# Kernel tuning notes

Measured on AMD Instinct MI355X. Metric: run time of the kernel, lower is better.

## Reference

```python
import jax, jax.numpy as jnp
import numpy as np

B, STATE, OBS = 131072, 16, 8


def _spd(key, b, n, scale=0.1):
    a = jax.random.normal(key, (b, n, n), dtype=jnp.float32) * scale
    return a @ jnp.swapaxes(a, -1, -2) + jnp.eye(n, dtype=jnp.float32)


def setup_inputs() -> dict:
    key = jax.random.key(0)
    ks = jax.random.split(key, 7)
    return {
        "input": jax.random.normal(ks[0], (B, OBS), dtype=jnp.float32),
        "mean": jax.random.normal(ks[1], (B, STATE), dtype=jnp.float32),
        "cov": _spd(ks[2], B, STATE),
        "H": jax.random.normal(ks[3], (B, OBS, STATE), dtype=jnp.float32) * 0.3,
        "R": _spd(ks[4], B, OBS),
        "F": jax.random.normal(ks[5], (B, STATE, STATE), dtype=jnp.float32) * 0.1,
        "Q": _spd(ks[6], B, STATE),
    }


def reference(input, mean, cov, H, R, F, Q):
    # ---- update (no NaNs in input, so the full-batch path is taken) ----
    Ht = jnp.swapaxes(H, -1, -2)                      # [B, s, o]
    S = H @ cov @ Ht + R                              # system covariance [B, o, o]
    PHt = cov @ Ht                                    # [B, s, o]
    # torch.solve(B, A) solves A X = B with A = S^T, B = (cov H^T)^T; K = X^T
    Kt = jnp.linalg.solve(jnp.swapaxes(S, -1, -2), jnp.swapaxes(PHt, -1, -2))
    K = jnp.swapaxes(Kt, -1, -2)                      # Kalman gain [B, s, o]
    resid = input - jnp.einsum('bos,bs->bo', H, mean)  # innovation [B, o]
    new_mean = mean + jnp.einsum('bso,bo->bs', K, resid)
    # Joseph-stabilized covariance update
    I = jnp.eye(cov.shape[-1], dtype=cov.dtype)
    p1 = I - K @ H                                    # [B, s, s]
    new_cov = p1 @ cov @ jnp.swapaxes(p1, -1, -2) + K @ R @ jnp.swapaxes(K, -1, -2)
    # ---- predict ----
    pred_mean = jnp.einsum('bij,bj->bi', F, new_mean)
    pred_cov = F @ new_cov @ jnp.swapaxes(F, -1, -2) + Q
    return pred_mean, pred_cov
```

## Files before the change

### kernel.cpp

```cpp
#include <hip/hip_runtime.h>
#include <math.h>


#define NB 131072
#define BPB 4
#define THREADS 64
#define LDS_PER 616

#define ROW_FMA16(acc, s, base) do {                                        \
    const float4* _r = (const float4*)(base);                               \
    float4 _c0=_r[0], _c1=_r[1], _c2=_r[2], _c3=_r[3];                      \
    acc[0]+=(s)*_c0.x; acc[1]+=(s)*_c0.y; acc[2]+=(s)*_c0.z; acc[3]+=(s)*_c0.w; \
    acc[4]+=(s)*_c1.x; acc[5]+=(s)*_c1.y; acc[6]+=(s)*_c1.z; acc[7]+=(s)*_c1.w; \
    acc[8]+=(s)*_c2.x; acc[9]+=(s)*_c2.y; acc[10]+=(s)*_c2.z; acc[11]+=(s)*_c2.w; \
    acc[12]+=(s)*_c3.x; acc[13]+=(s)*_c3.y; acc[14]+=(s)*_c3.z; acc[15]+=(s)*_c3.w; \
} while (0)

#define ROW_FMA8(acc, s, base) do {                                         \
    const float4* _r = (const float4*)(base);                               \
    float4 _c0=_r[0], _c1=_r[1];                                            \
    acc[0]+=(s)*_c0.x; acc[1]+=(s)*_c0.y; acc[2]+=(s)*_c0.z; acc[3]+=(s)*_c0.w; \
    acc[4]+=(s)*_c1.x; acc[5]+=(s)*_c1.y; acc[6]+=(s)*_c1.z; acc[7]+=(s)*_c1.w; \
} while (0)

__global__ void __launch_bounds__(THREADS, 4)
kalman_step_kernel(const float* __restrict__ input, const float* __restrict__ mean,
                   const float* __restrict__ cov, const float* __restrict__ H,
                   const float* __restrict__ R, const float* __restrict__ F,
                   const float* __restrict__ Q,
                   float* __restrict__ out_mean, float* __restrict__ out_cov)
{
    __shared__ __align__(16) float lds[BPB * LDS_PER];

    const int tid = threadIdx.x;
    const int g = tid >> 4;
    const int t = tid & 15;
    const long b = (long)blockIdx.x * BPB + g;

    float* Lb    = lds + g * LDS_PER;
    float* Mb    = Lb;
    float* Hb    = Lb + 256;
    float* Rb    = Lb + 384;
    float* Xb    = Lb + 448;
    float* meanv = Lb + 576;
    float* rn    = Lb + 592;

    float covrow[16];
    {
        const float4* C4 = (const float4*)(cov + b * 256 + t * 16);
        float4 c0 = C4[0], c1 = C4[1], c2 = C4[2], c3 = C4[3];
        covrow[0]=c0.x; covrow[1]=c0.y; covrow[2]=c0.z; covrow[3]=c0.w;
        covrow[4]=c1.x; covrow[5]=c1.y; covrow[6]=c1.z; covrow[7]=c1.w;
        covrow[8]=c2.x; covrow[9]=c2.y; covrow[10]=c2.z; covrow[11]=c2.w;
        covrow[12]=c3.x; covrow[13]=c3.y; covrow[14]=c3.z; covrow[15]=c3.w;
        float4* md = (float4*)(Mb + t * 16);
        md[0]=c0; md[1]=c1; md[2]=c2; md[3]=c3;
    }
    const float m = mean[b * 16 + t];
    meanv[t] = m;

    float hreg[16];
    float rreg[8];
    float inp = 0.0f;
    if (t < 8) {
        inp = input[b * 8 + t];
        const float4* H4 = (const float4*)(H + b * 128 + t * 16);
        float4 h0 = H4[0], h1 = H4[1], h2 = H4[2], h3 = H4[3];
        hreg[0]=h0.x; hreg[1]=h0.y; hreg[2]=h0.z; hreg[3]=h0.w;
        hreg[4]=h1.x; hreg[5]=h1.y; hreg[6]=h1.z; hreg[7]=h1.w;
        hreg[8]=h2.x; hreg[9]=h2.y; hreg[10]=h2.z; hreg[11]=h2.w;
        hreg[12]=h3.x; hreg[13]=h3.y; hreg[14]=h3.z; hreg[15]=h3.w;
        float4* hd = (float4*)(Hb + t * 16);
        hd[0]=h0; hd[1]=h1; hd[2]=h2; hd[3]=h3;
        const float4* R4 = (const float4*)(R + b * 64 + t * 8);
        float4 r0 = R4[0], r1 = R4[1];
        rreg[0]=r0.x; rreg[1]=r0.y; rreg[2]=r0.z; rreg[3]=r0.w;
        rreg[4]=r1.x; rreg[5]=r1.y; rreg[6]=r1.z; rreg[7]=r1.w;
        float4* rd = (float4*)(Rb + t * 8);
        rd[0]=r0; rd[1]=r1;
    }
    __syncthreads();

    float pht[8];
    #pragma unroll
    for (int o = 0; o < 8; ++o) {
        const float4* hr = (const float4*)(Hb + o * 16);
        float4 h0 = hr[0], h1 = hr[1], h2 = hr[2], h3 = hr[3];
        float acc;
        acc  = covrow[0]*h0.x + covrow[1]*h0.y + covrow[2]*h0.z + covrow[3]*h0.w;
        acc += covrow[4]*h1.x + covrow[5]*h1.y + covrow[6]*h1.z + covrow[7]*h1.w;
        acc += covrow[8]*h2.x + covrow[9]*h2.y + covrow[10]*h2.z + covrow[11]*h2.w;
        acc += covrow[12]*h3.x + covrow[13]*h3.y + covrow[14]*h3.z + covrow[15]*h3.w;
        pht[o] = acc;
    }
    {
        float4* pd = (float4*)(Xb + t * 8);
        pd[0] = make_float4(pht[0], pht[1], pht[2], pht[3]);
        pd[1] = make_float4(pht[4], pht[5], pht[6], pht[7]);
    }
    if (t < 8) {
        const float4* mv = (const float4*)meanv;
        float4 m0 = mv[0], m1 = mv[1], m2 = mv[2], m3 = mv[3];
        float acc = inp;
        acc -= hreg[0]*m0.x + hreg[1]*m0.y + hreg[2]*m0.z + hreg[3]*m0.w;
        acc -= hreg[4]*m1.x + hreg[5]*m1.y + hreg[6]*m1.z + hreg[7]*m1.w;
        acc -= hreg[8]*m2.x + hreg[9]*m2.y + hreg[10]*m2.z + hreg[11]*m2.w;
        acc -= hreg[12]*m3.x + hreg[13]*m3.y + hreg[14]*m3.z + hreg[15]*m3.w;
        rn[t] = acc;
    }
    __syncthreads();

    if (t < 8) {
        float sreg[8];
        #pragma unroll
        for (int c = 0; c < 8; ++c) sreg[c] = rreg[c];
        #pragma unroll
        for (int s = 0; s < 16; ++s) {
            float h = hreg[s];
            ROW_FMA8(sreg, h, Xb + s * 8);
        }
        float4* sd = (float4*)(Xb + t * 8);
        sd[0] = make_float4(sreg[0], sreg[1], sreg[2], sreg[3]);
        sd[1] = make_float4(sreg[4], sreg[5], sreg[6], sreg[7]);
    }
    __syncthreads();

    float Lm[8][8];
    #pragma unroll
    for (int i = 0; i < 8; ++i) {
        const float4* sr = (const float4*)(Xb + i * 8);
        float4 s0 = sr[0], s1 = sr[1];
        Lm[i][0]=s0.x; Lm[i][1]=s0.y; Lm[i][2]=s0.z; Lm[i][3]=s0.w;
        Lm[i][4]=s1.x; Lm[i][5]=s1.y; Lm[i][6]=s1.z; Lm[i][7]=s1.w;
    }
    float dinv[8];
    #pragma unroll
    for (int k = 0; k < 8; ++k) {
        float diag = Lm[k][k];
        #pragma unroll
        for (int j = 0; j < k; ++j) diag -= Lm[k][j] * Lm[k][j];
        float lkk = sqrtf(diag);
        float inv = 1.0f / lkk;
        dinv[k] = inv;
        #pragma unroll
        for (int i = k + 1; i < 8; ++i) {
            float v = Lm[i][k];
            #pragma unroll
            for (int j = 0; j < k; ++j) v -= Lm[i][j] * Lm[k][j];
            Lm[i][k] = v * inv;
        }
    }
    float yv[8];
    #pragma unroll
    for (int i = 0; i < 8; ++i) {
        float v = pht[i];
        #pragma unroll
        for (int j = 0; j < i; ++j) v -= Lm[i][j] * yv[j];
        yv[i] = v * dinv[i];
    }
    float Kr[8];
    #pragma unroll
    for (int i = 7; i >= 0; --i) {
        float v = yv[i];
        #pragma unroll
        for (int j = i + 1; j < 8; ++j) v -= Lm[j][i] * Kr[j];
        Kr[i] = v * dinv[i];
    }
    {
        const float4* rv = (const float4*)rn;
        float4 r0 = rv[0], r1 = rv[1];
        float nm = m;
        nm += Kr[0]*r0.x + Kr[1]*r0.y + Kr[2]*r0.z + Kr[3]*r0.w;
        nm += Kr[4]*r1.x + Kr[5]*r1.y + Kr[6]*r1.z + Kr[7]*r1.w;
        rn[t] = nm;
    }
    #pragma unroll
    for (int o = 0; o < 8; ++o) Xb[o * 16 + t] = Kr[o];
    __syncthreads();

    const float4* F4 = (const float4*)(F + b * 256 + t * 16);
    float4 fA = F4[0], fB = F4[1], fC = F4[2], fD = F4[3];

    float p1r[16];
    #pragma unroll
    for (int j = 0; j < 16; ++j) p1r[j] = (j == t) ? 1.0f : 0.0f;
    #pragma unroll
    for (int o = 0; o < 8; ++o) {
        float nko = -Kr[o];
        ROW_FMA16(p1r, nko, Hb + o * 16);
    }
    float KRr[8];
    #pragma unroll
    for (int c = 0; c < 8; ++c) KRr[c] = 0.0f;
    #pragma unroll
    for (int o = 0; o < 8; ++o) {
        float ko = Kr[o];
        ROW_FMA8(KRr, ko, Rb + o * 8);
    }

    float tmp[16];
    #pragma unroll
    for (int k = 0; k < 16; ++k) tmp[k] = 0.0f;
    #pragma unroll
    for (int j = 0; j < 16; ++j) {
        float pj = p1r[j];
        ROW_FMA16(tmp, pj, Mb + j * 16);
    }
    __syncthreads();
    #pragma unroll
    for (int k = 0; k < 16; ++k) Mb[k * 16 + t] = tmp[k];
    __syncthreads();

    const float4* Q4 = (const float4*)(Q + b * 256 + t * 16);
    float4 qA = Q4[0], qB = Q4[1], qC = Q4[2], qD = Q4[3];

    float nc[16];
    #pragma unroll
    for (int j = 0; j < 16; ++j) nc[j] = 0.0f;
    #pragma unroll
    for (int k = 0; k < 16; ++k) {
        float pk = p1r[k];
        ROW_FMA16(nc, pk, Mb + k * 16);
    }
    #pragma unroll
    for (int o = 0; o < 8; ++o) {
        float ko = KRr[o];
        ROW_FMA16(nc, ko, Xb + o * 16);
    }
    __syncthreads();
    {
        float4* md = (float4*)(Mb + t * 16);
        md[0] = make_float4(nc[0], nc[1], nc[2], nc[3]);
        md[1] = make_float4(nc[4], nc[5], nc[6], nc[7]);
        md[2] = make_float4(nc[8], nc[9], nc[10], nc[11]);
        md[3] = make_float4(nc[12], nc[13], nc[14], nc[15]);
    }
    __syncthreads();

    float freg[16];
    freg[0]=fA.x; freg[1]=fA.y; freg[2]=fA.z; freg[3]=fA.w;
    freg[4]=fB.x; freg[5]=fB.y; freg[6]=fB.z; freg[7]=fB.w;
    freg[8]=fC.x; freg[9]=fC.y; freg[10]=fC.z; freg[11]=fC.w;
    freg[12]=fD.x; freg[13]=fD.y; freg[14]=fD.z; freg[15]=fD.w;

    float fp[16];
    #pragma unroll
    for (int k = 0; k < 16; ++k) fp[k] = 0.0f;
    #pragma unroll
    for (int j = 0; j < 16; ++j) {
        float fj = freg[j];
        ROW_FMA16(fp, fj, Mb + j * 16);
    }
    float pm;
    {
        const float4* rv = (const float4*)rn;
        float4 r0 = rv[0], r1 = rv[1], r2 = rv[2], r3 = rv[3];
        pm  = freg[0]*r0.x + freg[1]*r0.y + freg[2]*r0.z + freg[3]*r0.w;
        pm += freg[4]*r1.x + freg[5]*r1.y + freg[6]*r1.z + freg[7]*r1.w;
        pm += freg[8]*r2.x + freg[9]*r2.y + freg[10]*r2.z + freg[11]*r2.w;
        pm += freg[12]*r3.x + freg[13]*r3.y + freg[14]*r3.z + freg[15]*r3.w;
    }
    __syncthreads();
    #pragma unroll
    for (int k = 0; k < 16; ++k) Mb[k * 16 + t] = fp[k];
    __syncthreads();

    float pc[16];
    pc[0]=qA.x; pc[1]=qA.y; pc[2]=qA.z; pc[3]=qA.w;
    pc[4]=qB.x; pc[5]=qB.y; pc[6]=qB.z; pc[7]=qB.w;
    pc[8]=qC.x; pc[9]=qC.y; pc[10]=qC.z; pc[11]=qC.w;
    pc[12]=qD.x; pc[13]=qD.y; pc[14]=qD.z; pc[15]=qD.w;
    #pragma unroll
    for (int k = 0; k < 16; ++k) {
        float fk = freg[k];
        ROW_FMA16(pc, fk, Mb + k * 16);
    }

    out_mean[b * 16 + t] = pm;
    {
        float4* od = (float4*)(out_cov + b * 256 + t * 16);
        od[0] = make_float4(pc[0], pc[1], pc[2], pc[3]);
        od[1] = make_float4(pc[4], pc[5], pc[6], pc[7]);
        od[2] = make_float4(pc[8], pc[9], pc[10], pc[11]);
        od[3] = make_float4(pc[12], pc[13], pc[14], pc[15]);
    }
}

extern "C" void kernel_launch(void* const* d_in, const int* in_sizes, int n_in,
                              void* d_out, int out_size, void* d_ws, size_t ws_size,
                              hipStream_t stream) {
    const float* input = (const float*)d_in[0];
    const float* mean  = (const float*)d_in[1];
    const float* cov   = (const float*)d_in[2];
    const float* H     = (const float*)d_in[3];
    const float* R     = (const float*)d_in[4];
    const float* F     = (const float*)d_in[5];
    const float* Q     = (const float*)d_in[6];
    float* out = (float*)d_out;
    float* out_mean = out;
    float* out_cov  = out + (size_t)NB * 16;

    dim3 grid(NB / BPB);
    dim3 block(THREADS);
    hipLaunchKernelGGL(kalman_step_kernel, grid, block, 0, stream,
                       input, mean, cov, H, R, F, Q, out_mean, out_cov);
}
```

Before: 486.1 us.

## Fold predict into update: compute F(I-KH) directly, drop Joseph intermediate stages

The covariance math is reassociated so that G = F(I-KH) = F - (FK)H and W = FK are built first. The result is then formed as G·P·Gᵀ + W·R·Wᵀ + Q, which removes the separate Joseph-form new_cov materialization and several LDS round trips and barriers. Cov and R are no longer staged in LDS, which shrinks the per-batch footprint, and the F load is hoisted earlier to overlap with the Cholesky solve. Outputs are written with nontemporal stores, and dot products are restructured into split partial sums. The reassociation changes rounding order slightly.

Measured after the change: 523.8 us. 1.08x slower.

```diff
diff --git a/kernel.cpp b/kernel.cpp
--- a/kernel.cpp
+++ b/kernel.cpp
@@ -5,7 +5,9 @@
 #define NB 131072
 #define BPB 4
 #define THREADS 64
-#define LDS_PER 616
+#define LDS_PER 552
+
+typedef float vf4 __attribute__((ext_vector_type(4)));
 
 #define ROW_FMA16(acc, s, base) do {                                        \
     const float4* _r = (const float4*)(base);                               \
@@ -23,6 +25,24 @@
     acc[4]+=(s)*_c1.x; acc[5]+=(s)*_c1.y; acc[6]+=(s)*_c1.z; acc[7]+=(s)*_c1.w; \
 } while (0)
 
+#define DOT16(res, v, base) do {                                            \
+    const float4* _r = (const float4*)(base);                               \
+    float4 _a=_r[0], _b=_r[1], _c=_r[2], _d=_r[3];                          \
+    float _s0 = v[0]*_a.x + v[1]*_a.y + v[2]*_a.z + v[3]*_a.w;              \
+    float _s1 = v[4]*_b.x + v[5]*_b.y + v[6]*_b.z + v[7]*_b.w;              \
+    float _s2 = v[8]*_c.x + v[9]*_c.y + v[10]*_c.z + v[11]*_c.w;            \
+    float _s3 = v[12]*_d.x + v[13]*_d.y + v[14]*_d.z + v[15]*_d.w;          \
+    res = (_s0+_s1)+(_s2+_s3);                                              \
+} while (0)
+
+#define DOT8(res, v, base) do {                                             \
+    const float4* _r = (const float4*)(base);                               \
+    float4 _a=_r[0], _b=_r[1];                                              \
+    float _s0 = v[0]*_a.x + v[1]*_a.y + v[2]*_a.z + v[3]*_a.w;              \
+    float _s1 = v[4]*_b.x + v[5]*_b.y + v[6]*_b.z + v[7]*_b.w;              \
+    res = _s0 + _s1;                                                        \
+} while (0)
+
 __global__ void __launch_bounds__(THREADS, 4)
 kalman_step_kernel(const float* __restrict__ input, const float* __restrict__ mean,
                    const float* __restrict__ cov, const float* __restrict__ H,
@@ -40,10 +60,9 @@
     float* Lb    = lds + g * LDS_PER;
     float* Mb    = Lb;
     float* Hb    = Lb + 256;
-    float* Rb    = Lb + 384;
-    float* Xb    = Lb + 448;
-    float* meanv = Lb + 576;
-    float* rn    = Lb + 592;
+    float* Xb    = Lb + 384;
+    float* meanv = Lb + 512;
+    float* rn    = Lb + 528;
 
     float covrow[16];
     {
@@ -53,8 +72,6 @@
         covrow[4]=c1.x; covrow[5]=c1.y; covrow[6]=c1.z; covrow[7]=c1.w;
         covrow[8]=c2.x; covrow[9]=c2.y; covrow[10]=c2.z; covrow[11]=c2.w;
         covrow[12]=c3.x; covrow[13]=c3.y; covrow[14]=c3.z; covrow[15]=c3.w;
-        float4* md = (float4*)(Mb + t * 16);
-        md[0]=c0; md[1]=c1; md[2]=c2; md[3]=c3;
     }
     const float m = mean[b * 16 + t];
     meanv[t] = m;
@@ -76,22 +93,13 @@
         float4 r0 = R4[0], r1 = R4[1];
         rreg[0]=r0.x; rreg[1]=r0.y; rreg[2]=r0.z; rreg[3]=r0.w;
         rreg[4]=r1.x; rreg[5]=r1.y; rreg[6]=r1.z; rreg[7]=r1.w;
-        float4* rd = (float4*)(Rb + t * 8);
-        rd[0]=r0; rd[1]=r1;
     }
     __syncthreads();
 
     float pht[8];
     #pragma unroll
     for (int o = 0; o < 8; ++o) {
-        const float4* hr = (const float4*)(Hb + o * 16);
-        float4 h0 = hr[0], h1 = hr[1], h2 = hr[2], h3 = hr[3];
-        float acc;
-        acc  = covrow[0]*h0.x + covrow[1]*h0.y + covrow[2]*h0.z + covrow[3]*h0.w;
-        acc += covrow[4]*h1.x + covrow[5]*h1.y + covrow[6]*h1.z + covrow[7]*h1.w;
-        acc += covrow[8]*h2.x + covrow[9]*h2.y + covrow[10]*h2.z + covrow[11]*h2.w;
-        acc += covrow[12]*h3.x + covrow[13]*h3.y + covrow[14]*h3.z + covrow[15]*h3.w;
-        pht[o] = acc;
+        DOT16(pht[o], covrow, Hb + o * 16);
     }
     {
         float4* pd = (float4*)(Xb + t * 8);
@@ -99,14 +107,9 @@
         pd[1] = make_float4(pht[4], pht[5], pht[6], pht[7]);
     }
     if (t < 8) {
-        const float4* mv = (const float4*)meanv;
-        float4 m0 = mv[0], m1 = mv[1], m2 = mv[2], m3 = mv[3];
-        float acc = inp;
-        acc -= hreg[0]*m0.x + hreg[1]*m0.y + hreg[2]*m0.z + hreg[3]*m0.w;
-        acc -= hreg[4]*m1.x + hreg[5]*m1.y + hreg[6]*m1.z + hreg[7]*m1.w;
-        acc -= hreg[8]*m2.x + hreg[9]*m2.y + hreg[10]*m2.z + hreg[11]*m2.w;
-        acc -= hreg[12]*m3.x + hreg[13]*m3.y + hreg[14]*m3.z + hreg[15]*m3.w;
-        rn[t] = acc;
+        float hm;
+        DOT16(hm, hreg, meanv);
+        rn[t] = inp - hm;
     }
     __syncthreads();
 
@@ -125,6 +128,9 @@
     }
     __syncthreads();
 
+    const float4* F4 = (const float4*)(F + b * 256 + t * 16);
+    float4 fA = F4[0], fB = F4[1], fC = F4[2], fD = F4[3];
+
     float Lm[8][8];
     #pragma unroll
     for (int i = 0; i < 8; ++i) {
@@ -174,66 +180,10 @@
         nm += Kr[4]*r1.x + Kr[5]*r1.y + Kr[6]*r1.z + Kr[7]*r1.w;
         rn[t] = nm;
     }
-    #pragma unroll
-    for (int o = 0; o < 8; ++o) Xb[o * 16 + t] = Kr[o];
-    __syncthreads();
-
-    const float4* F4 = (const float4*)(F + b * 256 + t * 16);
-    float4 fA = F4[0], fB = F4[1], fC = F4[2], fD = F4[3];
-
-    float p1r[16];
-    #pragma unroll
-    for (int j = 0; j < 16; ++j) p1r[j] = (j == t) ? 1.0f : 0.0f;
-    #pragma unroll
-    for (int o = 0; o < 8; ++o) {
-        float nko = -Kr[o];
-        ROW_FMA16(p1r, nko, Hb + o * 16);
-    }
-    float KRr[8];
-    #pragma unroll
-    for (int c = 0; c < 8; ++c) KRr[c] = 0.0f;
-    #pragma unroll
-    for (int o = 0; o < 8; ++o) {
-        float ko = Kr[o];
-        ROW_FMA8(KRr, ko, Rb + o * 8);
-    }
-
-    float tmp[16];
-    #pragma unroll
-    for (int k = 0; k < 16; ++k) tmp[k] = 0.0f;
-    #pragma unroll
-    for (int j = 0; j < 16; ++j) {
-        float pj = p1r[j];
-        ROW_FMA16(tmp, pj, Mb + j * 16);
-    }
-    __syncthreads();
-    #pragma unroll
-    for (int k = 0; k < 16; ++k) Mb[k * 16 + t] = tmp[k];
-    __syncthreads();
-
-    const float4* Q4 = (const float4*)(Q + b * 256 + t * 16);
-    float4 qA = Q4[0], qB = Q4[1], qC = Q4[2], qD = Q4[3];
-
-    float nc[16];
-    #pragma unroll
-    for (int j = 0; j < 16; ++j) nc[j] = 0.0f;
-    #pragma unroll
-    for (int k = 0; k < 16; ++k) {
-        float pk = p1r[k];
-        ROW_FMA16(nc, pk, Mb + k * 16);
-    }
-    #pragma unroll
-    for (int o = 0; o < 8; ++o) {
-        float ko = KRr[o];
-        ROW_FMA16(nc, ko, Xb + o * 16);
-    }
-    __syncthreads();
-    {
-        float4* md = (float4*)(Mb + t * 16);
-        md[0] = make_float4(nc[0], nc[1], nc[2], nc[3]);
-        md[1] = make_float4(nc[4], nc[5], nc[6], nc[7]);
-        md[2] = make_float4(nc[8], nc[9], nc[10], nc[11]);
-        md[3] = make_float4(nc[12], nc[13], nc[14], nc[15]);
+    {
+        float4* kd = (float4*)(Xb + t * 8);
+        kd[0] = make_float4(Kr[0], Kr[1], Kr[2], Kr[3]);
+        kd[1] = make_float4(Kr[4], Kr[5], Kr[6], Kr[7]);
     }
     __syncthreads();
 
@@ -243,26 +193,65 @@
     freg[8]=fC.x; freg[9]=fC.y; freg[10]=fC.z; freg[11]=fC.w;
     freg[12]=fD.x; freg[13]=fD.y; freg[14]=fD.z; freg[15]=fD.w;
 
-    float fp[16];
-    #pragma unroll
-    for (int k = 0; k < 16; ++k) fp[k] = 0.0f;
+    float Wr[8];
+    #pragma unroll
+    for (int c = 0; c < 8; ++c) Wr[c] = 0.0f;
     #pragma unroll
     for (int j = 0; j < 16; ++j) {
         float fj = freg[j];
-        ROW_FMA16(fp, fj, Mb + j * 16);
-    }
-    float pm;
-    {
-        const float4* rv = (const float4*)rn;
-        float4 r0 = rv[0], r1 = rv[1], r2 = rv[2], r3 = rv[3];
-        pm  = freg[0]*r0.x + freg[1]*r0.y + freg[2]*r0.z + freg[3]*r0.w;
-        pm += freg[4]*r1.x + freg[5]*r1.y + freg[6]*r1.z + freg[7]*r1.w;
-        pm += freg[8]*r2.x + freg[9]*r2.y + freg[10]*r2.z + freg[11]*r2.w;
-        pm += freg[12]*r3.x + freg[13]*r3.y + freg[14]*r3.z + freg[15]*r3.w;
-    }
-    __syncthreads();
-    #pragma unroll
-    for (int k = 0; k < 16; ++k) Mb[k * 16 + t] = fp[k];
+        ROW_FMA8(Wr, fj, Xb + j * 8);
+    }
+    {
+        float4* wd = (float4*)(Xb + t * 8);
+        wd[0] = make_float4(Wr[0], Wr[1], Wr[2], Wr[3]);
+        wd[1] = make_float4(Wr[4], Wr[5], Wr[6], Wr[7]);
+    }
+    float Gr[16];
+    #pragma unroll
+    for (int j = 0; j < 16; ++j) Gr[j] = freg[j];
+    #pragma unroll
+    for (int o = 0; o < 8; ++o) {
+        float nwo = -Wr[o];
+        ROW_FMA16(Gr, nwo, Hb + o * 16);
+    }
+    {
+        float4* gd = (float4*)(Mb + t * 16);
+        gd[0] = make_float4(Gr[0], Gr[1], Gr[2], Gr[3]);
+        gd[1] = make_float4(Gr[4], Gr[5], Gr[6], Gr[7]);
+        gd[2] = make_float4(Gr[8], Gr[9], Gr[10], Gr[11]);
+        gd[3] = make_float4(Gr[12], Gr[13], Gr[14], Gr[15]);
+    }
+    __syncthreads();
+
+    const float4* Q4 = (const float4*)(Q + b * 256 + t * 16);
+    float4 qA = Q4[0], qB = Q4[1], qC = Q4[2], qD = Q4[3];
+
+    float t2[16];
+    #pragma unroll
+    for (int c = 0; c < 16; ++c) {
+        DOT16(t2[c], covrow, Mb + c * 16);
+    }
+    {
+        float4* td = (float4*)(Mb + t * 16);
+        td[0] = make_float4(t2[0], t2[1], t2[2], t2[3]);
+        td[1] = make_float4(t2[4], t2[5], t2[6], t2[7]);
+        td[2] = make_float4(t2[8], t2[9], t2[10], t2[11]);
+        td[3] = make_float4(t2[12], t2[13], t2[14], t2[15]);
+    }
+    __syncthreads();
+
+    if (t < 8) {
+        float rw[16];
+        #pragma unroll
+        for (int c = 0; c < 16; ++c) {
+            DOT8(rw[c], rreg, Xb + c * 8);
+        }
+        float4* rd = (float4*)(Xb + t * 16);
+        rd[0] = make_float4(rw[0], rw[1], rw[2], rw[3]);
+        rd[1] = make_float4(rw[4], rw[5], rw[6], rw[7]);
+        rd[2] = make_float4(rw[8], rw[9], rw[10], rw[11]);
+        rd[3] = make_float4(rw[12], rw[13], rw[14], rw[15]);
+    }
     __syncthreads();
 
     float pc[16];
@@ -272,17 +261,28 @@
     pc[12]=qD.x; pc[13]=qD.y; pc[14]=qD.z; pc[15]=qD.w;
     #pragma unroll
     for (int k = 0; k < 16; ++k) {
-        float fk = freg[k];
-        ROW_FMA16(pc, fk, Mb + k * 16);
-    }
-
-    out_mean[b * 16 + t] = pm;
-    {
-        float4* od = (float4*)(out_cov + b * 256 + t * 16);
-        od[0] = make_float4(pc[0], pc[1], pc[2], pc[3]);
-        od[1] = make_float4(pc[4], pc[5], pc[6], pc[7]);
-        od[2] = make_float4(pc[8], pc[9], pc[10], pc[11]);
-        od[3] = make_float4(pc[12], pc[13], pc[14], pc[15]);
+        float gk = Gr[k];
+        ROW_FMA16(pc, gk, Mb + k * 16);
+    }
+    #pragma unroll
+    for (int o = 0; o < 8; ++o) {
+        float wo = Wr[o];
+        ROW_FMA16(pc, wo, Xb + o * 16);
+    }
+    float pm;
+    DOT16(pm, freg, rn);
+
+    __builtin_nontemporal_store(pm, &out_mean[b * 16 + t]);
+    {
+        vf4* od = (vf4*)(out_cov + b * 256 + t * 16);
+        vf4 v0 = {pc[0], pc[1], pc[2], pc[3]};
+        vf4 v1 = {pc[4], pc[5], pc[6], pc[7]};
+        vf4 v2 = {pc[8], pc[9], pc[10], pc[11]};
+        vf4 v3 = {pc[12], pc[13], pc[14], pc[15]};
+        __builtin_nontemporal_store(v0, od + 0);
+        __builtin_nontemporal_store(v1, od + 1);
+        __builtin_nontemporal_store(v2, od + 2);
+        __builtin_nontemporal_store(v3, od + 3);
     }
 }
 
```
